# Optimization experiments

Measured on AMD Instinct MI355X. Metric: run time of the kernel, lower is better.

Reference implementation:

```python
import jax, jax.numpy as jnp
import numpy as np

BITS = 4
GROUP = 128
IN_F = 4096
OUT_F = 4096
MASK = (1 << BITS) - 1  # 15
# non-uniform 4-bit codebook from QuantLinear (AF / AbnormalFloat style)
CODE = jnp.array([-6, -4, -3, -2, -1.5, -1, -0.5, -0.0,
                   0.0, 0.5, 1, 1.5, 2, 3, 4, 6], dtype=jnp.float32)


def setup_inputs() -> dict:
    key = jax.random.key(0)
    k1, k2, k3, k4, k5 = jax.random.split(key, 5)
    x = jax.random.normal(k1, (4, 2048, IN_F), dtype=jnp.float32)
    qweight = jax.random.randint(k2, (IN_F // 32 * BITS, OUT_F), 0, 2147483647, dtype=jnp.int32)
    n_groups = IN_F // GROUP
    scales = jax.random.uniform(k3, (n_groups, OUT_F), dtype=jnp.float32, minval=0.01, maxval=0.1)
    scales2 = jax.random.uniform(k4, (n_groups, OUT_F), dtype=jnp.float32, minval=0.01, maxval=0.1)
    bias = jax.random.normal(k5, (OUT_F,), dtype=jnp.float32)
    return {"x": x, "qweight": qweight, "scales": scales, "scales2": scales2, "bias": bias}


def dequantize(qweight, scales, scales2):
    # unpack: (rows, OUT) -> (rows, 8, OUT) nibbles; matches torch right_shift + & maxq
    wf = jnp.arange(0, 32, BITS, dtype=jnp.int32)          # (8,)
    q = (qweight[:, None, :] >> wf[None, :, None]) & MASK  # (IN/8, 8, OUT) ints in [0,15]
    q = q.reshape(IN_F // GROUP, GROUP, OUT_F)             # group-major layout
    w = CODE[q]                                            # codebook lookup
    # two-scale: positive codes use scales, negative codes use scales2 (per group, per out-col)
    w = jnp.where(w >= 0, w * scales[:, None, :], w * scales2[:, None, :])
    return w.reshape(IN_F, OUT_F)


def reference(x, qweight, scales, scales2, bias):
    W = dequantize(qweight, scales, scales2)        # (IN_F, OUT_F)
    out = jnp.einsum('bsi,io->bso', x, W) + bias    # grouped-dequant matmul + bias
    return out
```

## Files before the change

### kernel.cpp

```cpp
#include <hip/hip_runtime.h>
#include <hip/hip_bf16.h>
#include <stdint.h>

#define M_ROWS 8192
#define K_DIM  4096
#define N_DIM  4096

using bf16 = __hip_bfloat16;
typedef __attribute__((ext_vector_type(4))) float f32x4;
typedef __attribute__((ext_vector_type(8))) short s16x8;

__device__ __forceinline__ void gll16(const bf16* g, bf16* l) {
  __builtin_amdgcn_global_load_lds(
      (const __attribute__((address_space(1))) void*)g,
      (__attribute__((address_space(3))) void*)l, 16, 0, 0);
}

__global__ __launch_bounds__(256) void prep_k(
    const int* __restrict__ qw, const float* __restrict__ s1,
    const float* __restrict__ s2, const float* __restrict__ x,
    bf16* __restrict__ Bp, bf16* __restrict__ Ap)
{
  const int bid = blockIdx.x;
  if (bid < 2048) {
    const int t = bid * 256 + threadIdx.x;
    const int o = t & 4095;
    const int q = t >> 12;
    const int r0 = q << 2;
    const int g = r0 >> 4;
    const int nt = o >> 8, col = o & 255;
    const int kt = q >> 1, kh = q & 1;
    const int sw = (col >> 1) & 3;
    const float a = s1[g * 4096 + o] * 0.5f;
    const float b = s2[g * 4096 + o] * 0.5f;
    const uint64_t lo = 0x00FFFEFDFCFAF8F4ull;
    const uint64_t hi = 0x0C08060403020100ull;
    bf16* dst = Bp + (((size_t)((nt * 64 + kt) * 2 + kh)) << 13) + col * 32;
    #pragma unroll
    for (int j = 0; j < 4; ++j) {
      const uint32_t wbits = (uint32_t)qw[(size_t)(r0 + j) * 4096 + o];
      union { bf16 h[8]; s16x8 v; } u;
      #pragma unroll
      for (int i = 0; i < 8; ++i) {
        const int qc = (wbits >> (4 * i)) & 15;
        const uint64_t pk = (qc & 8) ? hi : lo;
        const int c2 = (int)(int8_t)(uint8_t)(pk >> ((qc & 7) * 8));
        const float sc = (qc & 8) ? a : b;
        u.h[i] = __float2bfloat16((float)c2 * sc);
      }
      *(s16x8*)(dst + ((j ^ sw) << 3)) = u.v;
    }
  } else {
    const int t = (bid - 2048) * 256 + threadIdx.x;
    const int s_lin = t & 3;
    const int kh = (t >> 2) & 1;
    const int kt = (t >> 3) & 63;
    const int m  = t >> 9;
    const int tm = m >> 8, row = m & 255;
    const float* s = x + (size_t)m * 4096 + (kt * 64 + kh * 32 + s_lin * 8);
    f32x4 v0 = *(const f32x4*)s;
    f32x4 v1 = *(const f32x4*)(s + 4);
    union { bf16 h[8]; s16x8 v; } u;
    #pragma unroll
    for (int j = 0; j < 4; ++j) {
      u.h[j]     = __float2bfloat16(v0[j]);
      u.h[4 + j] = __float2bfloat16(v1[j]);
    }
    const int ss = s_lin ^ ((row >> 1) & 3);
    bf16* dst = Ap + (((size_t)((tm * 64 + kt) * 2 + kh)) << 13) + row * 32 + ss * 8;
    *(s16x8*)dst = u.v;
  }
}

#define BAR()                                                         \
    asm volatile("s_barrier" ::: "memory");                           \
    __builtin_amdgcn_sched_barrier(0)

#define PH_SYNC()                                                     \
    asm volatile("s_barrier" ::: "memory");                           \
    asm volatile("s_waitcnt lgkmcnt(0)" ::: "memory");                \
    __builtin_amdgcn_sched_barrier(0)

#define VMW(N)                                                        \
    asm volatile("s_waitcnt vmcnt(" #N ")" ::: "memory");             \
    __builtin_amdgcn_sched_barrier(0)

#define MFMA16(MH)                                                    \
    __builtin_amdgcn_s_setprio(1);                                    \
    _Pragma("unroll")                                                 \
    for (int m = 0; m < 4; ++m) {                                     \
      _Pragma("unroll")                                               \
      for (int n = 0; n < 4; ++n)                                     \
        acc[(MH)*4+m][n] = __builtin_amdgcn_mfma_f32_16x16x32_bf16(   \
            af[m], bb[n], acc[(MH)*4+m][n], 0, 0, 0);                 \
    }                                                                 \
    __builtin_amdgcn_s_setprio(0)

#define KTILE(BUF, NK2, PRE, VM)                                      \
  {                                                                   \
    const bf16* A0_ = &lds[BUF][0][0];                                \
    const bf16* A1_ = &lds[BUF][1][0];                                \
    const bf16* B0_ = &lds[BUF][2][0];                                \
    const bf16* B1_ = &lds[BUF][3][0];                                \
                                                   \
    _Pragma("unroll")                                                 \
    for (int m = 0; m < 4; ++m) af[m] = *(const s16x8*)(A0_ + aoff + m * 512); \
    _Pragma("unroll")                                                 \
    for (int n = 0; n < 4; ++n) bb[n] = *(const s16x8*)(B0_ + boff + n * 512); \
    if (PRE) stage(Ab, (NK2), &lds[(BUF)^1][0][0]);                   \
    PH_SYNC();                                                        \
    MFMA16(0);                                                        \
                                                   \
    _Pragma("unroll")                                                 \
    for (int m = 0; m < 4; ++m) af[m] = *(const s16x8*)(A0_ + aoff + (m + 4) * 512); \
    if (PRE) stage(Bb, (NK2), &lds[(BUF)^1][2][0]);                   \
    PH_SYNC();                                                        \
    MFMA16(1);                                                        \
    VMW(VM);                                                          \
    BAR();                                                            \
                                                   \
    _Pragma("unroll")                                                 \
    for (int m = 0; m < 4; ++m) af[m] = *(const s16x8*)(A1_ + aoff + m * 512); \
    _Pragma("unroll")                                                 \
    for (int n = 0; n < 4; ++n) bb[n] = *(const s16x8*)(B1_ + boff + n * 512); \
    if (PRE) stage(Ab, (NK2) + 1, &lds[(BUF)^1][1][0]);               \
    PH_SYNC();                                                        \
    MFMA16(0);                                                        \
                                                   \
    _Pragma("unroll")                                                 \
    for (int m = 0; m < 4; ++m) af[m] = *(const s16x8*)(A1_ + aoff + (m + 4) * 512); \
    if (PRE) stage(Bb, (NK2) + 1, &lds[(BUF)^1][3][0]);               \
    PH_SYNC();                                                        \
    MFMA16(1);                                                        \
    VMW(VM);                                                          \
    BAR();                                                            \
  }

__global__ __launch_bounds__(512, 2) void gemm8_k(
    const bf16* __restrict__ Ap, const bf16* __restrict__ Bp,
    const float* __restrict__ bias, float* __restrict__ out)
{
  __shared__ bf16 lds[2][4][8192];

  const int id  = blockIdx.x;
  const int swz = (id & 7) * 64 + (id >> 3);
  const int tm  = swz >> 4;
  const int tn  = swz & 15;
  const int tid = (int)threadIdx.x;
  const int lane = tid & 63;
  const int w   = tid >> 6;
  const int wr  = w >> 2;
  const int wc  = w & 3;
  const int lr  = lane & 15;
  const int lg  = lane >> 4;
  const int sl  = (lg ^ ((lr >> 1) & 3)) << 3;
  const int aoff = (wr * 128 + lr) * 32 + sl;
  const int boff = (wc * 64 + lr) * 32 + sl;

  const bf16* Ab = Ap + ((size_t)tm << 20);
  const bf16* Bb = Bp + ((size_t)tn << 20);

  f32x4 acc[8][4];
  #pragma unroll
  for (int m = 0; m < 8; ++m)
    #pragma unroll
    for (int n = 0; n < 4; ++n) acc[m][n] = (f32x4){0.f, 0.f, 0.f, 0.f};

  auto stage = [&](const bf16* base, int c, bf16* dst) {
    const bf16* s = base + ((size_t)c << 13) + tid * 8;
    gll16(s, dst + tid * 8);
    gll16(s + 4096, dst + tid * 8 + 4096);
  };

  s16x8 af[4], bb[4];

  stage(Ab, 0, &lds[0][0][0]);
  stage(Bb, 0, &lds[0][2][0]);
  stage(Ab, 1, &lds[0][1][0]);
  stage(Bb, 1, &lds[0][3][0]);
  VMW(4);
  BAR();

  KTILE(0, 2, 1, 4);
  #pragma unroll 1
  for (int kt2 = 0; kt2 < 31; ++kt2) {
    KTILE(1, (4 * kt2 + 4), 1, 4);
    KTILE(0, (4 * kt2 + 6), 1, 4);
  }
  KTILE(1, 0, 0, 0);

  const int orow0 = tm * 256 + wr * 128 + lg * 4;
  const int ocol0 = tn * 256 + wc * 64 + lr;
  float bv[4];
  #pragma unroll
  for (int n = 0; n < 4; ++n) bv[n] = bias[ocol0 + n * 16];
  #pragma unroll
  for (int m = 0; m < 8; ++m) {
    #pragma unroll
    for (int r = 0; r < 4; ++r) {
      float* op = out + (size_t)(orow0 + m * 16 + r) * N_DIM + ocol0;
      #pragma unroll
      for (int n = 0; n < 4; ++n) op[n * 16] = acc[m][n][r] + bv[n];
    }
  }
}

__global__ __launch_bounds__(256) void dequant_f(
    const int* __restrict__ qw, const float* __restrict__ s1,
    const float* __restrict__ s2, bf16* __restrict__ Bp)
{
  const int t = blockIdx.x * 256 + threadIdx.x;
  const int o = t & 4095;
  const int r = t >> 12;
  const int g = r >> 4;
  const int kt = r >> 2;
  const int kk0 = (r & 3) * 8;
  const uint32_t wbits = (uint32_t)qw[(size_t)r * 4096 + o];
  const float a = s1[g * 4096 + o] * 0.5f;
  const float b = s2[g * 4096 + o] * 0.5f;
  const uint64_t lo = 0x00FFFEFDFCFAF8F4ull;
  const uint64_t hi = 0x0C08060403020100ull;
  union { bf16 h[8]; s16x8 v; } u;
  #pragma unroll
  for (int j = 0; j < 8; ++j) {
    const int q = (wbits >> (4 * j)) & 15;
    const uint64_t pk = (q & 8) ? hi : lo;
    const int c2 = (int)(int8_t)(uint8_t)(pk >> ((q & 7) * 8));
    const float s = (q & 8) ? a : b;
    u.h[j] = __float2bfloat16((float)c2 * s);
  }
  const int nt = o >> 7, col = o & 127;
  bf16* dst = Bp + (((size_t)(nt * 128 + kt) * 128 + col) * 32 + kk0);
  *(s16x8*)dst = u.v;
}

__global__ __launch_bounds__(256) void gemmf_k(
    const float* __restrict__ x, const bf16* __restrict__ Bp,
    const float* __restrict__ bias, float* __restrict__ out)
{
  __shared__ bf16 As[2][4096];
  __shared__ bf16 Bs[2][4096];

  const int id  = blockIdx.x;
  const int swz = (id & 7) * 256 + (id >> 3);
  const int tm  = swz >> 5;
  const int tn  = swz & 31;
  const int tid = threadIdx.x;
  const int lane = tid & 63;
  const int w   = tid >> 6;
  const int wr  = (w >> 1) * 64;
  const int wc  = (w & 1) * 64;
  const int lr  = lane & 15;
  const int lg  = lane >> 4;

  f32x4 acc[4][4];
  #pragma unroll
  for (int m = 0; m < 4; ++m)
    #pragma unroll
    for (int n = 0; n < 4; ++n) acc[m][n] = (f32x4){0.f, 0.f, 0.f, 0.f};

  const bf16* bsrc = Bp + ((size_t)tn << 19);
  const float* asrc_f = x + ((size_t)(tm * 128 + (tid >> 1)) << 12) + (tid & 1) * 16;
  float areg[16];

  auto stageB = [&](int kt, int buf) {
    const bf16* bs = bsrc + ((size_t)kt << 12);
    gll16(bs + tid * 8,        &Bs[buf][tid * 8]);
    gll16(bs + 2048 + tid * 8, &Bs[buf][2048 + tid * 8]);
  };
  auto loadA = [&](int kt) {
    const float* s = asrc_f + ((size_t)kt << 5);
    #pragma unroll
    for (int i = 0; i < 4; ++i)
      *(f32x4*)(areg + i * 4) = *(const f32x4*)(s + i * 4);
  };
  auto writeA = [&](int buf) {
    union { bf16 h[16]; s16x8 v[2]; } u;
    #pragma unroll
    for (int i = 0; i < 16; ++i) u.h[i] = __float2bfloat16(areg[i]);
    bf16* d = &As[buf][(tid >> 1) * 32 + (tid & 1) * 16];
    *(s16x8*)d = u.v[0];
    *(s16x8*)(d + 8) = u.v[1];
  };
  auto compute = [&](int buf) {
    s16x8 af[4], bv[4];
    #pragma unroll
    for (int m = 0; m < 4; ++m)
      af[m] = *(const s16x8*)(&As[buf][(wr + m * 16 + lr) * 32 + lg * 8]);
    #pragma unroll
    for (int n = 0; n < 4; ++n)
      bv[n] = *(const s16x8*)(&Bs[buf][(wc + n * 16 + lr) * 32 + lg * 8]);
    #pragma unroll
    for (int m = 0; m < 4; ++m)
      #pragma unroll
      for (int n = 0; n < 4; ++n)
        acc[m][n] = __builtin_amdgcn_mfma_f32_16x16x32_bf16(af[m], bv[n],
                                                            acc[m][n], 0, 0, 0);
  };

  stageB(0, 0);
  loadA(0);
  writeA(0);
  __syncthreads();

  #pragma unroll 2
  for (int kt = 0; kt < 128; ++kt) {
    const int buf = kt & 1;
    if (kt + 1 < 128) {
      stageB(kt + 1, buf ^ 1);
      loadA(kt + 1);
    }
    compute(buf);
    if (kt + 1 < 128) writeA(buf ^ 1);
    __syncthreads();
  }

  const int orow0 = tm * 128 + wr + lg * 4;
  const int ocol0 = tn * 128 + wc + lr;
  float bvv[4];
  #pragma unroll
  for (int n = 0; n < 4; ++n) bvv[n] = bias[ocol0 + n * 16];
  #pragma unroll
  for (int m = 0; m < 4; ++m) {
    #pragma unroll
    for (int r = 0; r < 4; ++r) {
      float* op = out + (size_t)(orow0 + m * 16 + r) * N_DIM + ocol0;
      #pragma unroll
      for (int n = 0; n < 4; ++n)
        op[n * 16] = acc[m][n][r] + bvv[n];
    }
  }
}

extern "C" void kernel_launch(void* const* d_in, const int* in_sizes, int n_in,
                              void* d_out, int out_size, void* d_ws, size_t ws_size,
                              hipStream_t stream) {
  const float* x    = (const float*)d_in[0];
  const int*   qw   = (const int*)d_in[1];
  const float* s1   = (const float*)d_in[2];
  const float* s2   = (const float*)d_in[3];
  const float* bias = (const float*)d_in[4];
  float* out = (float*)d_out;

  const size_t BP_BYTES = (size_t)K_DIM * N_DIM * 2;
  const size_t XB_BYTES = (size_t)M_ROWS * K_DIM * 2;
  bf16* Bp = (bf16*)d_ws;

  if (ws_size >= BP_BYTES + XB_BYTES) {
    bf16* Ap = (bf16*)((char*)d_ws + BP_BYTES);
    prep_k<<<dim3(18432), dim3(256), 0, stream>>>(qw, s1, s2, x, Bp, Ap);
    gemm8_k<<<dim3(512), dim3(512), 0, stream>>>(Ap, Bp, bias, out);
  } else {
    dequant_f<<<dim3(8192), dim3(256), 0, stream>>>(qw, s1, s2, Bp);
    gemmf_k<<<dim3(2048), dim3(256), 0, stream>>>(x, Bp, bias, out);
  }
}
```

Baseline: 265.9 us.

## Load B fragments directly from global into registers, bypassing LDS

The B operand tile is now read straight from global memory into double-buffered register fragments (bb0/bb1) instead of being staged through LDS. The prep kernel drops the LDS bank-conflict swizzle on B so each lane can read its fragment contiguously, and the LDS footprint halves to A only. Removing B's LDS reads and writes, and one barrier per k-tile, is meant to relieve LDS bandwidth and sync pressure. In exchange, each wave issues redundant global loads for B (the 2 wave-rows reload the same data), and there are 16 more live VGPRs per thread, which may affect occupancy at 2 blocks per CU.

```diff
diff --git a/kernel.cpp b/kernel.cpp
--- a/kernel.cpp
+++ b/kernel.cpp
@@ -30,7 +30,6 @@
     const int g = r0 >> 4;
     const int nt = o >> 8, col = o & 255;
     const int kt = q >> 1, kh = q & 1;
-    const int sw = (col >> 1) & 3;
     const float a = s1[g * 4096 + o] * 0.5f;
     const float b = s2[g * 4096 + o] * 0.5f;
     const uint64_t lo = 0x00FFFEFDFCFAF8F4ull;
@@ -48,7 +47,7 @@
         const float sc = (qc & 8) ? a : b;
         u.h[i] = __float2bfloat16((float)c2 * sc);
       }
-      *(s16x8*)(dst + ((j ^ sw) << 3)) = u.v;
+      *(s16x8*)(dst + (j << 3)) = u.v;
     }
   } else {
     const int t = (bid - 2048) * 256 + threadIdx.x;
@@ -85,54 +84,45 @@
     asm volatile("s_waitcnt vmcnt(" #N ")" ::: "memory");             \
     __builtin_amdgcn_sched_barrier(0)
 
-#define MFMA16(MH)                                                    \
+#define MFMA16(MH, BO, BARR)                                          \
     __builtin_amdgcn_s_setprio(1);                                    \
     _Pragma("unroll")                                                 \
     for (int m = 0; m < 4; ++m) {                                     \
       _Pragma("unroll")                                               \
       for (int n = 0; n < 4; ++n)                                     \
         acc[(MH)*4+m][n] = __builtin_amdgcn_mfma_f32_16x16x32_bf16(   \
-            af[m], bb[n], acc[(MH)*4+m][n], 0, 0, 0);                 \
+            af[m], BARR[(BO) + n], acc[(MH)*4+m][n], 0, 0, 0);        \
     }                                                                 \
     __builtin_amdgcn_s_setprio(0)
 
-#define KTILE(BUF, NK2, PRE, VM)                                      \
+#define KTILE(BUF, TN, PRE, BBC, BBN, WPUB)                           \
   {                                                                   \
     const bf16* A0_ = &lds[BUF][0][0];                                \
     const bf16* A1_ = &lds[BUF][1][0];                                \
-    const bf16* B0_ = &lds[BUF][2][0];                                \
-    const bf16* B1_ = &lds[BUF][3][0];                                \
                                                    \
     _Pragma("unroll")                                                 \
     for (int m = 0; m < 4; ++m) af[m] = *(const s16x8*)(A0_ + aoff + m * 512); \
-    _Pragma("unroll")                                                 \
-    for (int n = 0; n < 4; ++n) bb[n] = *(const s16x8*)(B0_ + boff + n * 512); \
-    if (PRE) stage(Ab, (NK2), &lds[(BUF)^1][0][0]);                   \
+    if (PRE) stage(Ab, (TN) * 2, &lds[(BUF)^1][0][0]);                \
     PH_SYNC();                                                        \
-    MFMA16(0);                                                        \
+    MFMA16(0, 0, BBC);                                                \
                                                    \
     _Pragma("unroll")                                                 \
     for (int m = 0; m < 4; ++m) af[m] = *(const s16x8*)(A0_ + aoff + (m + 4) * 512); \
-    if (PRE) stage(Bb, (NK2), &lds[(BUF)^1][2][0]);                   \
+    if (PRE) stage(Ab, (TN) * 2 + 1, &lds[(BUF)^1][1][0]);            \
     PH_SYNC();                                                        \
-    MFMA16(1);                                                        \
-    VMW(VM);                                                          \
-    BAR();                                                            \
+    MFMA16(1, 0, BBC);                                                \
                                                    \
     _Pragma("unroll")                                                 \
     for (int m = 0; m < 4; ++m) af[m] = *(const s16x8*)(A1_ + aoff + m * 512); \
-    _Pragma("unroll")                                                 \
-    for (int n = 0; n < 4; ++n) bb[n] = *(const s16x8*)(B1_ + boff + n * 512); \
-    if (PRE) stage(Ab, (NK2) + 1, &lds[(BUF)^1][1][0]);               \
+    if (PRE) loadB((TN), BBN);                                        \
     PH_SYNC();                                                        \
-    MFMA16(0);                                                        \
+    MFMA16(0, 4, BBC);                                                \
                                                    \
     _Pragma("unroll")                                                 \
     for (int m = 0; m < 4; ++m) af[m] = *(const s16x8*)(A1_ + aoff + (m + 4) * 512); \
-    if (PRE) stage(Bb, (NK2) + 1, &lds[(BUF)^1][3][0]);               \
     PH_SYNC();                                                        \
-    MFMA16(1);                                                        \
-    VMW(VM);                                                          \
+    MFMA16(1, 4, BBC);                                                \
+    VMW(WPUB);                                                        \
     BAR();                                                            \
   }
 
@@ -140,7 +130,7 @@
     const bf16* __restrict__ Ap, const bf16* __restrict__ Bp,
     const float* __restrict__ bias, float* __restrict__ out)
 {
-  __shared__ bf16 lds[2][4][8192];
+  __shared__ bf16 lds[2][2][8192];
 
   const int id  = blockIdx.x;
   const int swz = (id & 7) * 64 + (id >> 3);
@@ -155,7 +145,7 @@
   const int lg  = lane >> 4;
   const int sl  = (lg ^ ((lr >> 1) & 3)) << 3;
   const int aoff = (wr * 128 + lr) * 32 + sl;
-  const int boff = (wc * 64 + lr) * 32 + sl;
+  const int boffg = (wc * 64 + lr) * 32 + lg * 8;
 
   const bf16* Ab = Ap + ((size_t)tm << 20);
   const bf16* Bb = Bp + ((size_t)tn << 20);
@@ -171,23 +161,32 @@
     gll16(s, dst + tid * 8);
     gll16(s + 4096, dst + tid * 8 + 4096);
   };
-
-  s16x8 af[4], bb[4];
+  auto loadB = [&](int ktile, s16x8* d) {
+    const bf16* base = Bb + (((size_t)ktile * 2) << 13) + boffg;
+    #pragma unroll
+    for (int kh = 0; kh < 2; ++kh)
+      #pragma unroll
+      for (int n = 0; n < 4; ++n)
+        d[kh * 4 + n] = *(const s16x8*)(base + (kh << 13) + n * 512);
+  };
+
+  s16x8 af[4];
+  s16x8 bb0[8], bb1[8];
 
   stage(Ab, 0, &lds[0][0][0]);
-  stage(Bb, 0, &lds[0][2][0]);
   stage(Ab, 1, &lds[0][1][0]);
-  stage(Bb, 1, &lds[0][3][0]);
-  VMW(4);
+  __builtin_amdgcn_sched_barrier(0);
+  loadB(0, bb0);
+  VMW(8);
   BAR();
 
-  KTILE(0, 2, 1, 4);
+  KTILE(0, 1, 1, bb0, bb1, 8);
   #pragma unroll 1
   for (int kt2 = 0; kt2 < 31; ++kt2) {
-    KTILE(1, (4 * kt2 + 4), 1, 4);
-    KTILE(0, (4 * kt2 + 6), 1, 4);
-  }
-  KTILE(1, 0, 0, 0);
+    KTILE(1, (2 * kt2 + 2), 1, bb1, bb0, 8);
+    KTILE(0, (2 * kt2 + 3), 1, bb0, bb1, 8);
+  }
+  KTILE(1, 0, 0, bb1, bb0, 0);
 
   const int orow0 = tm * 256 + wr * 128 + lg * 4;
   const int ocol0 = tn * 256 + wc * 64 + lr;
```

Measured after the change: 303.7 us. 1.14x slower.

## Switch GEMM to 128x256 tiles with triple-buffered LDS and XCD-aware mapping

Applied to the files above, without the earlier changes.

Shrinks the block tile from 256x256 to 128x256, doubles the grid to 1024 blocks, and raises the occupancy hint to 4 blocks per CU. The LDS pipeline becomes a three-stage ring of single K-chunks instead of two double-width buffers. The A-prep layout is changed to match the new tile, and block-to-tile mapping groups M tiles per XCD for L2 reuse. The aim is better latency hiding and load balance across CUs, at the cost of lower arithmetic intensity per block and more re-reads of B.

```diff
diff --git a/kernel.cpp b/kernel.cpp
--- a/kernel.cpp
+++ b/kernel.cpp
@@ -29,13 +29,12 @@
     const int r0 = q << 2;
     const int g = r0 >> 4;
     const int nt = o >> 8, col = o & 255;
-    const int kt = q >> 1, kh = q & 1;
     const int sw = (col >> 1) & 3;
     const float a = s1[g * 4096 + o] * 0.5f;
     const float b = s2[g * 4096 + o] * 0.5f;
     const uint64_t lo = 0x00FFFEFDFCFAF8F4ull;
     const uint64_t hi = 0x0C08060403020100ull;
-    bf16* dst = Bp + (((size_t)((nt * 64 + kt) * 2 + kh)) << 13) + col * 32;
+    bf16* dst = Bp + (((size_t)(nt * 128 + q)) << 13) + col * 32;
     #pragma unroll
     for (int j = 0; j < 4; ++j) {
       const uint32_t wbits = (uint32_t)qw[(size_t)(r0 + j) * 4096 + o];
@@ -52,12 +51,12 @@
     }
   } else {
     const int t = (bid - 2048) * 256 + threadIdx.x;
-    const int s_lin = t & 3;
-    const int kh = (t >> 2) & 1;
-    const int kt = (t >> 3) & 63;
+    const int k8 = t & 511;
+    const int kt = k8 >> 2;
+    const int s_lin = k8 & 3;
     const int m  = t >> 9;
-    const int tm = m >> 8, row = m & 255;
-    const float* s = x + (size_t)m * 4096 + (kt * 64 + kh * 32 + s_lin * 8);
+    const int tm = m >> 7, row = m & 127;
+    const float* s = x + (size_t)m * 4096 + k8 * 8;
     f32x4 v0 = *(const f32x4*)s;
     f32x4 v1 = *(const f32x4*)(s + 4);
     union { bf16 h[8]; s16x8 v; } u;
@@ -67,7 +66,7 @@
       u.h[4 + j] = __float2bfloat16(v1[j]);
     }
     const int ss = s_lin ^ ((row >> 1) & 3);
-    bf16* dst = Ap + (((size_t)((tm * 64 + kt) * 2 + kh)) << 13) + row * 32 + ss * 8;
+    bf16* dst = Ap + (((size_t)(tm * 128 + kt)) << 12) + row * 32 + ss * 8;
     *(s16x8*)dst = u.v;
   }
 }
@@ -85,67 +84,38 @@
     asm volatile("s_waitcnt vmcnt(" #N ")" ::: "memory");             \
     __builtin_amdgcn_sched_barrier(0)
 
-#define MFMA16(MH)                                                    \
+#define KT9(BUF, KTN, PRE, VM)                                        \
+  {                                                                   \
+    const bf16* L_ = &lds[BUF][0];                                    \
+    _Pragma("unroll")                                                 \
+    for (int m = 0; m < 4; ++m) af[m] = *(const s16x8*)(L_ + aoff + m * 512); \
+    _Pragma("unroll")                                                 \
+    for (int n = 0; n < 4; ++n) bb[n] = *(const s16x8*)(L_ + boff + n * 512); \
+    if (PRE) stage((KTN), ((BUF) + 2) % 3);                           \
+    PH_SYNC();                                                        \
     __builtin_amdgcn_s_setprio(1);                                    \
     _Pragma("unroll")                                                 \
     for (int m = 0; m < 4; ++m) {                                     \
       _Pragma("unroll")                                               \
       for (int n = 0; n < 4; ++n)                                     \
-        acc[(MH)*4+m][n] = __builtin_amdgcn_mfma_f32_16x16x32_bf16(   \
-            af[m], bb[n], acc[(MH)*4+m][n], 0, 0, 0);                 \
+        acc[m][n] = __builtin_amdgcn_mfma_f32_16x16x32_bf16(          \
+            af[m], bb[n], acc[m][n], 0, 0, 0);                        \
     }                                                                 \
-    __builtin_amdgcn_s_setprio(0)
-
-#define KTILE(BUF, NK2, PRE, VM)                                      \
-  {                                                                   \
-    const bf16* A0_ = &lds[BUF][0][0];                                \
-    const bf16* A1_ = &lds[BUF][1][0];                                \
-    const bf16* B0_ = &lds[BUF][2][0];                                \
-    const bf16* B1_ = &lds[BUF][3][0];                                \
-                                                   \
-    _Pragma("unroll")                                                 \
-    for (int m = 0; m < 4; ++m) af[m] = *(const s16x8*)(A0_ + aoff + m * 512); \
-    _Pragma("unroll")                                                 \
-    for (int n = 0; n < 4; ++n) bb[n] = *(const s16x8*)(B0_ + boff + n * 512); \
-    if (PRE) stage(Ab, (NK2), &lds[(BUF)^1][0][0]);                   \
-    PH_SYNC();                                                        \
-    MFMA16(0);                                                        \
-                                                   \
-    _Pragma("unroll")                                                 \
-    for (int m = 0; m < 4; ++m) af[m] = *(const s16x8*)(A0_ + aoff + (m + 4) * 512); \
-    if (PRE) stage(Bb, (NK2), &lds[(BUF)^1][2][0]);                   \
-    PH_SYNC();                                                        \
-    MFMA16(1);                                                        \
+    __builtin_amdgcn_s_setprio(0);                                    \
     VMW(VM);                                                          \
     BAR();                                                            \
-                                                   \
-    _Pragma("unroll")                                                 \
-    for (int m = 0; m < 4; ++m) af[m] = *(const s16x8*)(A1_ + aoff + m * 512); \
-    _Pragma("unroll")                                                 \
-    for (int n = 0; n < 4; ++n) bb[n] = *(const s16x8*)(B1_ + boff + n * 512); \
-    if (PRE) stage(Ab, (NK2) + 1, &lds[(BUF)^1][1][0]);               \
-    PH_SYNC();                                                        \
-    MFMA16(0);                                                        \
-                                                   \
-    _Pragma("unroll")                                                 \
-    for (int m = 0; m < 4; ++m) af[m] = *(const s16x8*)(A1_ + aoff + (m + 4) * 512); \
-    if (PRE) stage(Bb, (NK2) + 1, &lds[(BUF)^1][3][0]);               \
-    PH_SYNC();                                                        \
-    MFMA16(1);                                                        \
-    VMW(VM);                                                          \
-    BAR();                                                            \
-  }
-
-__global__ __launch_bounds__(512, 2) void gemm8_k(
+  }
+
+__global__ __launch_bounds__(512, 4) void gemm9_k(
     const bf16* __restrict__ Ap, const bf16* __restrict__ Bp,
     const float* __restrict__ bias, float* __restrict__ out)
 {
-  __shared__ bf16 lds[2][4][8192];
+  __shared__ bf16 lds[3][12288];
 
   const int id  = blockIdx.x;
-  const int swz = (id & 7) * 64 + (id >> 3);
-  const int tm  = swz >> 4;
-  const int tn  = swz & 15;
+  const int xcd = id & 7, lid = id >> 3;
+  const int tn  = lid >> 3;
+  const int tm  = xcd * 8 + (lid & 7);
   const int tid = (int)threadIdx.x;
   const int lane = tid & 63;
   const int w   = tid >> 6;
@@ -154,48 +124,48 @@
   const int lr  = lane & 15;
   const int lg  = lane >> 4;
   const int sl  = (lg ^ ((lr >> 1) & 3)) << 3;
-  const int aoff = (wr * 128 + lr) * 32 + sl;
-  const int boff = (wc * 64 + lr) * 32 + sl;
-
-  const bf16* Ab = Ap + ((size_t)tm << 20);
-  const bf16* Bb = Bp + ((size_t)tn << 20);
-
-  f32x4 acc[8][4];
-  #pragma unroll
-  for (int m = 0; m < 8; ++m)
+  const int aoff = (wr * 64 + lr) * 32 + sl;
+  const int boff = 4096 + (wc * 64 + lr) * 32 + sl;
+
+  const bf16* Abase = Ap + ((size_t)tm << 19);
+  const bf16* Bbase = Bp + ((size_t)tn << 20);
+
+  f32x4 acc[4][4];
+  #pragma unroll
+  for (int m = 0; m < 4; ++m)
     #pragma unroll
     for (int n = 0; n < 4; ++n) acc[m][n] = (f32x4){0.f, 0.f, 0.f, 0.f};
 
-  auto stage = [&](const bf16* base, int c, bf16* dst) {
-    const bf16* s = base + ((size_t)c << 13) + tid * 8;
-    gll16(s, dst + tid * 8);
-    gll16(s + 4096, dst + tid * 8 + 4096);
+  auto stage = [&](int kt, int buf) {
+    gll16(Abase + ((size_t)kt << 12) + tid * 8, &lds[buf][tid * 8]);
+    const bf16* bs = Bbase + ((size_t)kt << 13) + tid * 8;
+    gll16(bs,        &lds[buf][4096 + tid * 8]);
+    gll16(bs + 4096, &lds[buf][8192 + tid * 8]);
   };
 
   s16x8 af[4], bb[4];
 
-  stage(Ab, 0, &lds[0][0][0]);
-  stage(Bb, 0, &lds[0][2][0]);
-  stage(Ab, 1, &lds[0][1][0]);
-  stage(Bb, 1, &lds[0][3][0]);
-  VMW(4);
+  stage(0, 0);
+  stage(1, 1);
+  VMW(3);
   BAR();
 
-  KTILE(0, 2, 1, 4);
   #pragma unroll 1
-  for (int kt2 = 0; kt2 < 31; ++kt2) {
-    KTILE(1, (4 * kt2 + 4), 1, 4);
-    KTILE(0, (4 * kt2 + 6), 1, 4);
-  }
-  KTILE(1, 0, 0, 0);
-
-  const int orow0 = tm * 256 + wr * 128 + lg * 4;
+  for (int t3 = 0; t3 < 42; ++t3) {
+    KT9(0, 3 * t3 + 2, 1, 3);
+    KT9(1, 3 * t3 + 3, 1, 3);
+    KT9(2, 3 * t3 + 4, 1, 3);
+  }
+  KT9(0, 0, 0, 0);
+  KT9(1, 0, 0, 0);
+
+  const int orow0 = tm * 128 + wr * 64 + lg * 4;
   const int ocol0 = tn * 256 + wc * 64 + lr;
   float bv[4];
   #pragma unroll
   for (int n = 0; n < 4; ++n) bv[n] = bias[ocol0 + n * 16];
   #pragma unroll
-  for (int m = 0; m < 8; ++m) {
+  for (int m = 0; m < 4; ++m) {
     #pragma unroll
     for (int r = 0; r < 4; ++r) {
       float* op = out + (size_t)(orow0 + m * 16 + r) * N_DIM + ocol0;
@@ -349,7 +319,7 @@
   if (ws_size >= BP_BYTES + XB_BYTES) {
     bf16* Ap = (bf16*)((char*)d_ws + BP_BYTES);
     prep_k<<<dim3(18432), dim3(256), 0, stream>>>(qw, s1, s2, x, Bp, Ap);
-    gemm8_k<<<dim3(512), dim3(512), 0, stream>>>(Ap, Bp, bias, out);
+    gemm9_k<<<dim3(1024), dim3(512), 0, stream>>>(Ap, Bp, bias, out);
   } else {
     dequant_f<<<dim3(8192), dim3(256), 0, stream>>>(qw, s1, s2, Bp);
     gemmf_k<<<dim3(2048), dim3(256), 0, stream>>>(x, Bp, bias, out);
```

Result: no change. 271.0 us (+1.9%).
